# Performance work log

Hardware: AMD Instinct MI355X
Metric: run time of the kernel (lower is better)

## Reference

```python
import jax, jax.numpy as jnp
import numpy as np

B, N, M, C, S = 4, 16384, 128, 128, 512  # batch, points, boxes, feat dim, sampled pts


def setup_inputs() -> dict:
    key = jax.random.key(0)
    k1, k2, k3, k4, k5, k6, k7 = jax.random.split(key, 7)
    # point cloud roughly in a LiDAR extent
    xy = jax.random.uniform(k1, (B, N, 2), minval=-50.0, maxval=50.0)
    z = jax.random.uniform(k2, (B, N, 1), minval=-3.0, maxval=3.0)
    points = jnp.concatenate([xy, z], axis=-1).astype(jnp.float32)
    point_features = jax.random.normal(k3, (B, N, C), dtype=jnp.float32)
    # boxes: (cx, cy, cz_bottom, dx, dy, dz, rz)
    ctr_xy = jax.random.uniform(k4, (B, M, 2), minval=-50.0, maxval=50.0)
    ctr_z = jax.random.uniform(k5, (B, M, 1), minval=-3.0, maxval=0.0)
    sizes = jax.random.uniform(k6, (B, M, 3), minval=2.0, maxval=8.0)
    rz = jax.random.uniform(k7, (B, M, 1), minval=-np.pi, maxval=np.pi)
    boxes3d = jnp.concatenate([ctr_xy, ctr_z, sizes, rz], axis=-1).astype(jnp.float32)
    return {"points": points, "point_features": point_features, "boxes3d": boxes3d}


def _pool_one_box(points, feats, box):
    # points (N,3), feats (N,C), box (7,)
    n = points.shape[0]
    cx, cy, cz, dx, dy, dz, rz = box
    cz = cz + 0.5 * dz  # bottom center -> geometric center (mmcv convention)
    sx = points[:, 0] - cx
    sy = points[:, 1] - cy
    cosa = jnp.cos(-rz)
    sina = jnp.sin(-rz)
    lx = sx * cosa - sy * sina
    ly = sx * sina + sy * cosa
    mask = (
        (jnp.abs(points[:, 2] - cz) <= 0.5 * dz)
        & (lx > -0.5 * dx) & (lx < 0.5 * dx)
        & (ly > -0.5 * dy) & (ly < 0.5 * dy)
    )
    cnt = mask.sum(dtype=jnp.int32)
    # rank of each in-box point among in-box points (first-come order)
    rank = jnp.cumsum(mask.astype(jnp.int32)) - 1
    pos = jnp.where(mask, rank, n)  # out-of-range for non-members -> dropped
    table = jnp.zeros((n,), jnp.int32).at[pos].set(
        jnp.arange(n, dtype=jnp.int32), mode="drop")
    # wrap-around duplication when cnt < S (kernel copies k % cnt)
    j = jnp.arange(S, dtype=jnp.int32) % jnp.maximum(cnt, 1)
    idx = table[j]  # (S,)
    pooled = jnp.concatenate([points[idx], feats[idx]], axis=-1)  # (S, 3+C)
    pooled = jnp.where(cnt > 0, pooled, jnp.zeros_like(pooled))
    empty = (cnt == 0).astype(jnp.int32)
    return pooled, empty


def reference(points, point_features, boxes3d):
    # vmap over boxes, then over batch
    per_scene = jax.vmap(_pool_one_box, in_axes=(None, None, 0))
    per_batch = jax.vmap(per_scene, in_axes=(0, 0, 0))
    pooled_features, pooled_empty_flag = per_batch(points, point_features, boxes3d)
    return pooled_features, pooled_empty_flag
```

## Files before the change

kernel.cpp:

```cpp
#include <hip/hip_runtime.h>

#define B_ 4
#define N_ 16384
#define M_ 128
#define C_ 128
#define S_ 512
#define ROW_ 131
#define NCHUNK_ 256
#define KBOX_ 4

typedef float f4_t __attribute__((ext_vector_type(4)));

__global__ __launch_bounds__(256) void mask_kernel(
    const float* __restrict__ points,
    const float* __restrict__ boxes,
    unsigned long long* __restrict__ masks)
{
    const int gwave = blockIdx.x * 4 + (threadIdx.x >> 6);
    const int lane  = threadIdx.x & 63;
    const int grp   = gwave >> 4;
    const int seg   = gwave & 15;
    const int bm0   = grp * KBOX_;
    const int b     = bm0 >> 7;

    const float* pb = points + (size_t)b * N_ * 3;
    float px[16], py[16], pz[16];
    #pragma unroll
    for (int k = 0; k < 16; ++k) {
        const int i = (seg * 16 + k) * 64 + lane;
        px[k] = pb[i*3+0]; py[k] = pb[i*3+1]; pz[k] = pb[i*3+2];
    }

    for (int kb = 0; kb < KBOX_; ++kb) {
        const int bm = bm0 + kb;
        const float* bx = boxes + bm * 7;
        const float cx = bx[0], cy = bx[1], czb = bx[2];
        const float dx = bx[3], dy = bx[4], dzv = bx[5], rz = bx[6];
        const float cz   = __fadd_rn(czb, __fmul_rn(0.5f, dzv));
        const float cosa = (float)cos(-(double)rz);
        const float sina = (float)sin(-(double)rz);
        const float hdx = 0.5f * dx, hdy = 0.5f * dy, hdz = 0.5f * dzv;

        #pragma unroll
        for (int k = 0; k < 16; ++k) {
            const float sx = __fsub_rn(px[k], cx);
            const float sy = __fsub_rn(py[k], cy);
            const float lx = __fsub_rn(__fmul_rn(sx, cosa), __fmul_rn(sy, sina));
            const float ly = __fadd_rn(__fmul_rn(sx, sina), __fmul_rn(sy, cosa));
            const bool pred = (fabsf(__fsub_rn(pz[k], cz)) <= hdz) &&
                              (lx > -hdx) && (lx < hdx) &&
                              (ly > -hdy) && (ly < hdy);
            const unsigned long long m = __ballot(pred);
            if (lane == 0) masks[(size_t)bm * NCHUNK_ + seg * 16 + k] = m;
        }
    }
}

__global__ __launch_bounds__(1024, 8) void pool_kernel(
    const float* __restrict__ points,
    const float* __restrict__ feats,
    const unsigned long long* __restrict__ masks,
    float* __restrict__ out,
    float* __restrict__ flags_out)
{
    const int bm   = blockIdx.x;
    const int b    = bm >> 7;
    const int tid  = threadIdx.x;
    const int lane = tid & 63;

    __shared__ int  s_wsum[4];
    __shared__ int  s_idx[S_];
    __shared__ f4_t rowtab[S_ + 1];

    int total;
    if (tid < 256) {
        const int w = tid >> 6;
        const unsigned long long m0 = masks[(size_t)bm * NCHUNK_ + tid];
        const int c = __popcll(m0);

        int incl = c;
        #pragma unroll
        for (int d = 1; d < 64; d <<= 1) {
            const int t = __shfl_up(incl, d, 64);
            if (lane >= d) incl += t;
        }
        if (lane == 63) s_wsum[w] = incl;
        __syncthreads();
        const int w0 = s_wsum[0], w1 = s_wsum[1], w2 = s_wsum[2], w3 = s_wsum[3];
        const int woff  = (w > 0 ? w0 : 0) + (w > 1 ? w1 : 0) + (w > 2 ? w2 : 0);
        total = w0 + w1 + w2 + w3;
        const int P = incl - c + woff;

        if (c > 0 && P < S_) {
            unsigned long long m = m0;
            int pos = P;
            while (m && pos < S_) {
                const int bit = __ffsll((unsigned long long)m) - 1;
                m &= m - 1;
                s_idx[pos++] = tid * 64 + bit;
            }
        }
    } else {
        __syncthreads();
        total = s_wsum[0] + s_wsum[1] + s_wsum[2] + s_wsum[3];
    }
    __syncthreads();

    const int cnt_eff = total < S_ ? total : S_;
    const int denom   = cnt_eff > 0 ? cnt_eff : 1;

    if (total > 0) {
        for (int s = tid; s <= S_; s += 1024) {
            const int j   = (s < S_) ? ((unsigned)s % (unsigned)denom) : 0;
            const int idx = s_idx[j];
            const size_t pb = (size_t)b * N_ + (unsigned)idx;
            f4_t r;
            r[0] = __int_as_float(idx * C_);
            r[1] = points[pb * 3 + 0];
            r[2] = points[pb * 3 + 1];
            r[3] = points[pb * 3 + 2];
            rowtab[s] = r;
        }
    }
    __syncthreads();

    float* ob = out + (size_t)bm * (S_ * ROW_);
    if (total == 0) {
        const f4_t z = {0.0f, 0.0f, 0.0f, 0.0f};
        for (int f = tid; f < (S_ * ROW_) / 4; f += 1024)
            *(f4_t*)(ob + 4 * f) = z;
    } else {
        const float* fb = feats + (size_t)b * N_ * C_;
        for (int f = tid; f < (S_ * ROW_) / 4; f += 1024) {
            const int e = 4 * f;
            const unsigned s0 = (unsigned)e / (unsigned)ROW_;
            const int col0 = e - (int)s0 * ROW_;
            const f4_t ra = rowtab[s0];
            const f4_t rb = rowtab[s0 + 1];
            f4_t v;
            #pragma unroll
            for (int jj = 0; jj < 4; ++jj) {
                int col = col0 + jj;
                const bool cross = col >= ROW_;
                col = cross ? col - ROW_ : col;
                const f4_t r = cross ? rb : ra;
                const int coff = col < 3 ? 0 : col - 3;
                const float fv = fb[__float_as_int(r[0]) + coff];
                v[jj] = col == 0 ? r[1] : col == 1 ? r[2] : col == 2 ? r[3] : fv;
            }
            *(f4_t*)(ob + e) = v;
        }
    }
    if (tid == 0) flags_out[bm] = (total == 0) ? 1.0f : 0.0f;
}

extern "C" void kernel_launch(void* const* d_in, const int* in_sizes, int n_in,
                              void* d_out, int out_size, void* d_ws, size_t ws_size,
                              hipStream_t stream) {
    const float* points = (const float*)d_in[0];
    const float* feats  = (const float*)d_in[1];
    const float* boxes  = (const float*)d_in[2];
    float* out = (float*)d_out;

    unsigned long long* masks = (unsigned long long*)d_ws;

    float* flags = out + (size_t)B_ * M_ * S_ * ROW_;

    mask_kernel<<<B_ * M_ * 16 / 4 / KBOX_, 256, 0, stream>>>(
        points, boxes, masks);
    pool_kernel<<<B_ * M_, 1024, 0, stream>>>(points, feats, masks, out, flags);
}
```

Measured before the change: 182.5 us.

## Split pool kernel into four 256-thread blocks per box with row-per-wave copies

The pool kernel now launches four 256-thread blocks per box instead of one 1024-thread block. Each block recomputes the mask prefix scan and writes a quarter of the output rows. The gather changes from flat float4 output chunks with per-element column decoding to one wave per output row, writing scalar stores at lane offsets. This drops the division/select logic and the rowtab packing in exchange for redundant scan work, unaligned scalar stores on 131-float rows, and a small xyz staging table.

```diff
diff --git a/kernel.cpp b/kernel.cpp
--- a/kernel.cpp
+++ b/kernel.cpp
@@ -56,102 +56,87 @@
     }
 }
 
-__global__ __launch_bounds__(1024, 8) void pool_kernel(
+__global__ __launch_bounds__(256, 4) void pool_kernel(
     const float* __restrict__ points,
     const float* __restrict__ feats,
     const unsigned long long* __restrict__ masks,
     float* __restrict__ out,
     float* __restrict__ flags_out)
 {
-    const int bm   = blockIdx.x;
+    const int blk  = blockIdx.x;
+    const int bm   = blk >> 2;
+    const int q    = blk & 3;
     const int b    = bm >> 7;
     const int tid  = threadIdx.x;
+    const int w    = tid >> 6;
     const int lane = tid & 63;
 
-    __shared__ int  s_wsum[4];
-    __shared__ int  s_idx[S_];
-    __shared__ f4_t rowtab[S_ + 1];
+    __shared__ int   s_wsum[4];
+    __shared__ int   s_idx[S_];
+    __shared__ float s_xyz[S_ * 3];
 
-    int total;
-    if (tid < 256) {
-        const int w = tid >> 6;
-        const unsigned long long m0 = masks[(size_t)bm * NCHUNK_ + tid];
-        const int c = __popcll(m0);
+    const unsigned long long m0 = masks[(size_t)bm * NCHUNK_ + tid];
+    const int c = __popcll(m0);
+    int incl = c;
+    #pragma unroll
+    for (int d = 1; d < 64; d <<= 1) {
+        const int t = __shfl_up(incl, d, 64);
+        if (lane >= d) incl += t;
+    }
+    if (lane == 63) s_wsum[w] = incl;
+    __syncthreads();
+    const int w0 = s_wsum[0], w1 = s_wsum[1], w2 = s_wsum[2], w3 = s_wsum[3];
+    const int woff  = (w > 0 ? w0 : 0) + (w > 1 ? w1 : 0) + (w > 2 ? w2 : 0);
+    const int total = w0 + w1 + w2 + w3;
+    int pos = incl - c + woff;
 
-        int incl = c;
-        #pragma unroll
-        for (int d = 1; d < 64; d <<= 1) {
-            const int t = __shfl_up(incl, d, 64);
-            if (lane >= d) incl += t;
+    if (c > 0 && pos < S_) {
+        unsigned long long m = m0;
+        while (m && pos < S_) {
+            const int bit = __ffsll((unsigned long long)m) - 1;
+            m &= m - 1;
+            s_idx[pos++] = tid * 64 + bit;
         }
-        if (lane == 63) s_wsum[w] = incl;
-        __syncthreads();
-        const int w0 = s_wsum[0], w1 = s_wsum[1], w2 = s_wsum[2], w3 = s_wsum[3];
-        const int woff  = (w > 0 ? w0 : 0) + (w > 1 ? w1 : 0) + (w > 2 ? w2 : 0);
-        total = w0 + w1 + w2 + w3;
-        const int P = incl - c + woff;
-
-        if (c > 0 && P < S_) {
-            unsigned long long m = m0;
-            int pos = P;
-            while (m && pos < S_) {
-                const int bit = __ffsll((unsigned long long)m) - 1;
-                m &= m - 1;
-                s_idx[pos++] = tid * 64 + bit;
-            }
-        }
-    } else {
-        __syncthreads();
-        total = s_wsum[0] + s_wsum[1] + s_wsum[2] + s_wsum[3];
     }
     __syncthreads();
 
     const int cnt_eff = total < S_ ? total : S_;
     const int denom   = cnt_eff > 0 ? cnt_eff : 1;
 
-    if (total > 0) {
-        for (int s = tid; s <= S_; s += 1024) {
-            const int j   = (s < S_) ? ((unsigned)s % (unsigned)denom) : 0;
-            const int idx = s_idx[j];
-            const size_t pb = (size_t)b * N_ + (unsigned)idx;
-            f4_t r;
-            r[0] = __int_as_float(idx * C_);
-            r[1] = points[pb * 3 + 0];
-            r[2] = points[pb * 3 + 1];
-            r[3] = points[pb * 3 + 2];
-            rowtab[s] = r;
-        }
+    float* ob = out + (size_t)bm * (S_ * ROW_);
+
+    if (total == 0) {
+        for (int t = tid; t < 128 * ROW_; t += 256)
+            ob[q * (128 * ROW_) + t] = 0.0f;
+        if (q == 0 && tid == 0) flags_out[bm] = 1.0f;
+        return;
+    }
+
+    for (int t = tid; t < cnt_eff; t += 256) {
+        const size_t pbase = ((size_t)b * N_ + (unsigned)s_idx[t]) * 3;
+        s_xyz[t*3+0] = points[pbase+0];
+        s_xyz[t*3+1] = points[pbase+1];
+        s_xyz[t*3+2] = points[pbase+2];
     }
     __syncthreads();
 
-    float* ob = out + (size_t)bm * (S_ * ROW_);
-    if (total == 0) {
-        const f4_t z = {0.0f, 0.0f, 0.0f, 0.0f};
-        for (int f = tid; f < (S_ * ROW_) / 4; f += 1024)
-            *(f4_t*)(ob + 4 * f) = z;
-    } else {
-        const float* fb = feats + (size_t)b * N_ * C_;
-        for (int f = tid; f < (S_ * ROW_) / 4; f += 1024) {
-            const int e = 4 * f;
-            const unsigned s0 = (unsigned)e / (unsigned)ROW_;
-            const int col0 = e - (int)s0 * ROW_;
-            const f4_t ra = rowtab[s0];
-            const f4_t rb = rowtab[s0 + 1];
-            f4_t v;
-            #pragma unroll
-            for (int jj = 0; jj < 4; ++jj) {
-                int col = col0 + jj;
-                const bool cross = col >= ROW_;
-                col = cross ? col - ROW_ : col;
-                const f4_t r = cross ? rb : ra;
-                const int coff = col < 3 ? 0 : col - 3;
-                const float fv = fb[__float_as_int(r[0]) + coff];
-                v[jj] = col == 0 ? r[1] : col == 1 ? r[2] : col == 2 ? r[3] : fv;
-            }
-            *(f4_t*)(ob + e) = v;
-        }
+    const float* fb = feats + (size_t)b * N_ * C_;
+    const int s0 = q * 128 + w * 32;
+    #pragma unroll 4
+    for (int k = 0; k < 32; ++k) {
+        const int s = s0 + k;
+        const int j = (int)((unsigned)s % (unsigned)denom);
+        const int idx = s_idx[j];
+        const float* fr = fb + (size_t)(unsigned)idx * C_;
+        const float a  = (lane < 3) ? s_xyz[j*3 + lane] : fr[lane - 3];
+        const float d2 = fr[61 + lane];
+        const float d3 = (lane < 3) ? fr[125 + lane] : 0.0f;
+        float* orow = ob + s * ROW_;
+        orow[lane]      = a;
+        orow[64 + lane] = d2;
+        if (lane < 3) orow[128 + lane] = d3;
     }
-    if (tid == 0) flags_out[bm] = (total == 0) ? 1.0f : 0.0f;
+    if (q == 0 && tid == 0) flags_out[bm] = 0.0f;
 }
 
 extern "C" void kernel_launch(void* const* d_in, const int* in_sizes, int n_in,
@@ -168,5 +153,5 @@
 
     mask_kernel<<<B_ * M_ * 16 / 4 / KBOX_, 256, 0, stream>>>(
         points, boxes, masks);
-    pool_kernel<<<B_ * M_, 1024, 0, stream>>>(points, feats, masks, out, flags);
+    pool_kernel<<<B_ * M_ * 4, 256, 0, stream>>>(points, feats, masks, out, flags);
 }
```

New measurement: 198.8 us. 1.09x slower.
